# Kernel tuning notes

Hardware: AMD Instinct MI355X
Metric: run time of the kernel (lower is better)

## Reference

```python
import jax, jax.numpy as jnp
import numpy as np

NEURON_CDECAY = 0.5
NEURON_VDECAY = 0.75
NEURON_VTH = 0.5
SPIKE_PSEUDO_GRAD_WINDOW = 0.5

@jax.custom_vjp
def pseudo_spike(v):
    return (v > NEURON_VTH).astype(v.dtype)

def _ps_fwd(v):
    return pseudo_spike(v), v

def _ps_bwd(v, g):
    return (g * (jnp.abs(v - NEURON_VTH) < SPIKE_PSEUDO_GRAD_WINDOW).astype(g.dtype),)

pseudo_spike.defvjp(_ps_fwd, _ps_bwd)

def conv1d(x, w, b):
    # x: (B, Cin, L), w: (Cout, Cin, K), stride 2, VALID padding
    y = jax.lax.conv_general_dilated(x, w, window_strides=(2,), padding='VALID',
                                     dimension_numbers=('NCH', 'OIH', 'NCH'))
    return y + b[None, :, None]

def neuron(syn_out, u, v, s):
    u = u * NEURON_CDECAY + syn_out
    v = v * NEURON_VDECAY * (1.0 - s) + u
    s = pseudo_spike(v)
    return u, v, s

def setup_inputs() -> dict:
    key = jax.random.key(0)
    ks = jax.random.split(key, 18)
    B, T, L = 4096, 50, 360
    h1, h2, h3, A = 256, 256, 128, 2
    def w(k, shape, fan_in):
        bound = 1.0 / np.sqrt(fan_in)
        return jax.random.uniform(k, shape, jnp.float32, -bound, bound)
    return {
        'normal_spikes': (jax.random.uniform(ks[0], (B, 6, T)) < 0.5).astype(jnp.float32),
        'scan_spikes': (jax.random.uniform(ks[1], (B, 1, L, T)) < 0.5).astype(jnp.float32),
        'batch_size': B,
        'conv1_w': w(ks[2], (5, 1, 5), 5),   'conv1_b': w(ks[3], (5,), 5),
        'conv2_w': w(ks[4], (5, 5, 5), 25),  'conv2_b': w(ks[5], (5,), 25),
        'conv3_w': w(ks[6], (5, 5, 5), 25),  'conv3_b': w(ks[7], (5,), 25),
        'fc1_w': w(ks[8], (h1, 216), 216),   'fc1_b': w(ks[9], (h1,), 216),
        'fc2_w': w(ks[10], (h2, h1), h1),    'fc2_b': w(ks[11], (h2,), h1),
        'fc3_w': w(ks[12], (h3, h2), h2),    'fc3_b': w(ks[13], (h3,), h2),
        'fc4_w': w(ks[14], (A, h3), h3),     'fc4_b': w(ks[15], (A,), h3),
    }

def reference(normal_spikes, scan_spikes, batch_size,
              conv1_w, conv1_b, conv2_w, conv2_b, conv3_w, conv3_b,
              fc1_w, fc1_b, fc2_w, fc2_b, fc3_w, fc3_b, fc4_w, fc4_b):
    B = batch_size
    T = normal_spikes.shape[-1]
    A = fc4_w.shape[0]
    # time-major sequences for lax.scan
    scan_seq = jnp.moveaxis(scan_spikes, -1, 0)    # (T, B, 1, 360)
    norm_seq = jnp.moveaxis(normal_spikes, -1, 0)  # (T, B, 6)

    z = lambda *s: jnp.zeros(s, jnp.float32)
    init = (
        (z(B, 5, 178), z(B, 5, 178), z(B, 5, 178)),
        (z(B, 5, 87),  z(B, 5, 87),  z(B, 5, 87)),
        (z(B, 5, 42),  z(B, 5, 42),  z(B, 5, 42)),
        (z(B, 256), z(B, 256), z(B, 256)),
        (z(B, 256), z(B, 256), z(B, 256)),
        (z(B, 128), z(B, 128), z(B, 128)),
        (z(B, A),   z(B, A),   z(B, A)),
        z(B, A),
    )

    def step(carry, xs):
        c1, c2, c3, f1, f2, f3, f4, acc = carry
        scan_x, norm_x = xs
        c1 = neuron(conv1d(scan_x, conv1_w, conv1_b), *c1)
        c2 = neuron(conv1d(c1[2], conv2_w, conv2_b), *c2)
        c3 = neuron(conv1d(c2[2], conv3_w, conv3_b), *c3)
        comb = jnp.concatenate([c3[2].reshape(B, -1), norm_x], axis=1)  # (B, 216)
        f1 = neuron(comb @ fc1_w.T + fc1_b, *f1)
        f2 = neuron(f1[2] @ fc2_w.T + fc2_b, *f2)
        f3 = neuron(f2[2] @ fc3_w.T + fc3_b, *f3)
        f4 = neuron(f3[2] @ fc4_w.T + fc4_b, *f4)
        acc = acc + f4[2]
        return (c1, c2, c3, f1, f2, f3, f4, acc), None

    carry, _ = jax.lax.scan(step, init, (scan_seq, norm_seq))
    return carry[-1] / T
```

## Files before the change

### kernel.cpp

```cpp
#include <hip/hip_runtime.h>
#include <cstdint>
#include <cstddef>


#define NB 4096

__device__ __forceinline__ void neuron_update(float syn, float& u, float& v, float& s) {
    u = u * 0.5f + syn;
    v = v * 0.75f * (1.0f - s) + u;
    s = (v > 0.5f) ? 1.0f : 0.0f;
}

__global__ __launch_bounds__(192) void conv1_kernel(
    const float* __restrict__ x, const float* __restrict__ w1,
    const float* __restrict__ b1, unsigned long long* __restrict__ S1)
{
    __shared__ float xl[9000];
    const int tid = threadIdx.x;
    const int b = blockIdx.x;
    const int j = tid;
    const int lbase = (j < 178) ? 2 * j : 354;

    float wr[25], br[5];
#pragma unroll
    for (int q = 0; q < 25; ++q) wr[q] = w1[q];
#pragma unroll
    for (int o = 0; o < 5; ++o) br[o] = b1[o];

    float u[5], v[5], s[5];
#pragma unroll
    for (int o = 0; o < 5; ++o) { u[o] = 0.f; v[o] = 0.f; s[o] = 0.f; }

    const float* xb = x + (size_t)b * 18000;
    for (int half = 0; half < 2; ++half) {
        const int t0 = half * 25;
        __syncthreads();
        for (int e = tid; e < 9000; e += 192)
            xl[e] = xb[(e / 25) * 50 + t0 + (e % 25)];
        __syncthreads();
        for (int dt = 0; dt < 25; ++dt) {
            const int t = t0 + dt;
            float xv[5];
#pragma unroll
            for (int k = 0; k < 5; ++k) xv[k] = xl[(lbase + k) * 25 + dt];
#pragma unroll
            for (int o = 0; o < 5; ++o) {
                float syn = 0.f;
#pragma unroll
                for (int k = 0; k < 5; ++k) syn += wr[o * 5 + k] * xv[k];
                syn += br[o];
                neuron_update(syn, u[o], v[o], s[o]);
                unsigned long long m = __ballot(j < 178 && s[o] > 0.5f);
                if ((tid & 63) == 0)
                    S1[(((size_t)b * 50 + t) * 5 + o) * 3 + (tid >> 6)] = m;
            }
        }
    }
}

__global__ __launch_bounds__(128) void conv2_kernel(
    const unsigned int* __restrict__ S1, const float* __restrict__ w2,
    const float* __restrict__ b2, unsigned int* __restrict__ S2)
{
    __shared__ unsigned int s1l[1501];
    const int tid = threadIdx.x;
    const int b = blockIdx.x;

    float wr[125], br[5];
#pragma unroll
    for (int q = 0; q < 125; ++q) wr[q] = w2[q];
#pragma unroll
    for (int o = 0; o < 5; ++o) br[o] = b2[o];

    const unsigned int* src = S1 + (size_t)b * 1500;
    for (int e = tid; e < 1500; e += 128) s1l[e] = src[e];
    __syncthreads();

    const int p = (tid < 87) ? 2 * tid : 172;
    const int pw = p >> 5, ps = p & 31;

    float u[5], v[5], s[5];
#pragma unroll
    for (int o = 0; o < 5; ++o) { u[o] = 0.f; v[o] = 0.f; s[o] = 0.f; }

    for (int t = 0; t < 50; ++t) {
        float xv[25];
#pragma unroll
        for (int ci = 0; ci < 5; ++ci) {
            const int base = (t * 5 + ci) * 6 + pw;
            unsigned long long bits =
                ((((unsigned long long)s1l[base + 1]) << 32) | (unsigned long long)s1l[base]) >> ps;
#pragma unroll
            for (int k = 0; k < 5; ++k)
                xv[ci * 5 + k] = ((bits >> k) & 1ULL) ? 1.0f : 0.0f;
        }
#pragma unroll
        for (int o = 0; o < 5; ++o) {
            float syn = 0.f;
#pragma unroll
            for (int q = 0; q < 25; ++q) syn += wr[o * 25 + q] * xv[q];
            syn += br[o];
            neuron_update(syn, u[o], v[o], s[o]);
            unsigned long long m = __ballot(tid < 87 && s[o] > 0.5f);
            const size_t outb = (((size_t)b * 50 + t) * 5 + o) * 3;
            if (tid == 0) {
                S2[outb]     = (unsigned int)m;
                S2[outb + 1] = (unsigned int)(m >> 32);
            }
            if (tid == 64) S2[outb + 2] = (unsigned int)m;
        }
    }
}

__global__ __launch_bounds__(64) void conv3_kernel(
    const unsigned int* __restrict__ S2, const float* __restrict__ w3,
    const float* __restrict__ b3, const float* __restrict__ normal,
    unsigned long long* __restrict__ S3)
{
    __shared__ unsigned int s2l[751];
    const int tid = threadIdx.x;
    const int b = blockIdx.x;

    float wr[125], br[5];
#pragma unroll
    for (int q = 0; q < 125; ++q) wr[q] = w3[q];
#pragma unroll
    for (int o = 0; o < 5; ++o) br[o] = b3[o];

    const unsigned int* src = S2 + (size_t)b * 750;
    for (int e = tid; e < 750; e += 64) s2l[e] = src[e];
    __syncthreads();

    const int p = (tid < 42) ? 2 * tid : 82;
    const int pw = p >> 5, ps = p & 31;

    float u[5], v[5], s[5];
#pragma unroll
    for (int o = 0; o < 5; ++o) { u[o] = 0.f; v[o] = 0.f; s[o] = 0.f; }

    for (int t = 0; t < 50; ++t) {
        float xv[25];
#pragma unroll
        for (int ci = 0; ci < 5; ++ci) {
            const int base = (t * 5 + ci) * 3 + pw;
            unsigned long long bits =
                ((((unsigned long long)s2l[base + 1]) << 32) | (unsigned long long)s2l[base]) >> ps;
#pragma unroll
            for (int k = 0; k < 5; ++k)
                xv[ci * 5 + k] = ((bits >> k) & 1ULL) ? 1.0f : 0.0f;
        }
        unsigned long long m[5];
#pragma unroll
        for (int o = 0; o < 5; ++o) {
            float syn = 0.f;
#pragma unroll
            for (int q = 0; q < 25; ++q) syn += wr[o * 25 + q] * xv[q];
            syn += br[o];
            neuron_update(syn, u[o], v[o], s[o]);
            m[o] = __ballot(tid < 42 && s[o] > 0.5f);
        }
        const unsigned long long nm =
            __ballot(tid < 6 && normal[((size_t)b * 6 + tid) * 50 + t] > 0.5f);
        if (tid == 0) {
            unsigned long long r0 = m[0] | (m[1] << 42);
            unsigned long long r1 = (m[1] >> 22) | (m[2] << 20) | (m[3] << 62);
            unsigned long long r2 = (m[3] >> 2) | (m[4] << 40);
            unsigned long long r3 = (m[4] >> 24) | (nm << 18);
            unsigned long long* dst = S3 + ((size_t)b * 50 + t) * 4;
            dst[0] = r0; dst[1] = r1; dst[2] = r2; dst[3] = r3;
        }
    }
}

__global__ __launch_bounds__(256, 2) void exact_gemm_kernel(
    const uint32_t* __restrict__ bits,
    const float* __restrict__ W,
    const float* __restrict__ bias,
    float* __restrict__ syn,
    int Ntot, int KREAL, int KT, int row0)
{
    __shared__ __align__(16) float a_lds[32 * 256];
    __shared__ __align__(16) float b_lds[32 * 128];

    const int tid = threadIdx.x;
    const int m0 = blockIdx.x * 256;
    const int nbase = blockIdx.y * 128;
    const int tm = tid & 15, tn = tid >> 4;

    const uint32_t* myBits = bits + (size_t)(row0 + m0 + tid) * 8;
    const int awBase = ((((tid >> 2) & 3) << 4) | (tid >> 4)) * 4 + (tid & 3);

    const int bn = tid & 127;
    const int bk0 = (tid >> 7) * 16;
    const float* wRow = W + (size_t)(nbase + bn) * KREAL;

    float acc[16][8];
#pragma unroll
    for (int j = 0; j < 16; ++j)
#pragma unroll
        for (int r = 0; r < 8; ++r) acc[j][r] = 0.f;

    for (int kt = 0; kt < KT; ++kt) {
        const int k0 = kt * 32;

        const uint32_t wbits = myBits[kt];
        float4 bq[4];
#pragma unroll
        for (int i = 0; i < 4; ++i) {
            const int k = k0 + bk0 + i * 4;
            if (k + 3 < KREAL) {
                bq[i] = *reinterpret_cast<const float4*>(&wRow[k]);
            } else {
                float x = 0.f, y = 0.f, z = 0.f, w = 0.f;
                if (k     < KREAL) x = wRow[k];
                if (k + 1 < KREAL) y = wRow[k + 1];
                if (k + 2 < KREAL) z = wRow[k + 2];
                if (k + 3 < KREAL) w = wRow[k + 3];
                bq[i] = make_float4(x, y, z, w);
            }
        }

        __syncthreads();

#pragma unroll
        for (int kk = 0; kk < 32; ++kk)
            a_lds[kk * 256 + awBase] = ((wbits >> kk) & 1u) ? 1.0f : 0.0f;
#pragma unroll
        for (int i = 0; i < 4; ++i) {
            b_lds[(bk0 + i * 4 + 0) * 128 + bn] = bq[i].x;
            b_lds[(bk0 + i * 4 + 1) * 128 + bn] = bq[i].y;
            b_lds[(bk0 + i * 4 + 2) * 128 + bn] = bq[i].z;
            b_lds[(bk0 + i * 4 + 3) * 128 + bn] = bq[i].w;
        }
        __syncthreads();

#pragma unroll 2
        for (int kk = 0; kk < 32; ++kk) {
            float a[16];
#pragma unroll
            for (int iq = 0; iq < 4; ++iq) {
                const float4 av = *reinterpret_cast<const float4*>(
                    &a_lds[kk * 256 + (iq * 16 + tm) * 4]);
                a[iq * 4 + 0] = av.x; a[iq * 4 + 1] = av.y;
                a[iq * 4 + 2] = av.z; a[iq * 4 + 3] = av.w;
            }
            float bf[8];
            const float4 b0 = *reinterpret_cast<const float4*>(
                &b_lds[kk * 128 + tn * 8]);
            const float4 b1 = *reinterpret_cast<const float4*>(
                &b_lds[kk * 128 + tn * 8 + 4]);
            bf[0] = b0.x; bf[1] = b0.y; bf[2] = b0.z; bf[3] = b0.w;
            bf[4] = b1.x; bf[5] = b1.y; bf[6] = b1.z; bf[7] = b1.w;
#pragma unroll
            for (int j = 0; j < 16; ++j)
#pragma unroll
                for (int r = 0; r < 8; ++r)
                    acc[j][r] += a[j] * bf[r];
        }
    }

#pragma unroll
    for (int j = 0; j < 16; ++j) {
        const int m = m0 + tm * 16 + j;
        float* so = syn + (size_t)m * Ntot + nbase + tn * 8;
        float4 o0, o1;
        o0.x = acc[j][0] + bias[nbase + tn * 8 + 0];
        o0.y = acc[j][1] + bias[nbase + tn * 8 + 1];
        o0.z = acc[j][2] + bias[nbase + tn * 8 + 2];
        o0.w = acc[j][3] + bias[nbase + tn * 8 + 3];
        o1.x = acc[j][4] + bias[nbase + tn * 8 + 4];
        o1.y = acc[j][5] + bias[nbase + tn * 8 + 5];
        o1.z = acc[j][6] + bias[nbase + tn * 8 + 6];
        o1.w = acc[j][7] + bias[nbase + tn * 8 + 7];
        *reinterpret_cast<float4*>(so) = o0;
        *reinterpret_cast<float4*>(so + 4) = o1;
    }
}

template <int N>
__global__ __launch_bounds__(256) void fc_scan_kernel(
    const float* __restrict__ syn, unsigned long long* __restrict__ SF, int b0)
{
    const int tid = threadIdx.x;
    const int wid = blockIdx.x * 4 + (tid >> 6);
    const int lane = tid & 63;
    constexpr int OB = N / 64;
    const int bl = wid / OB;
    const int ob = wid - bl * OB;
    const int o = ob * 64 + lane;

    float u = 0.f, v = 0.f, s = 0.f;
    for (int t = 0; t < 50; ++t) {
        const float sv = syn[((size_t)bl * 50 + t) * N + o];
        neuron_update(sv, u, v, s);
        const unsigned long long m = __ballot(s > 0.5f);
        if (lane == 0) SF[((size_t)(b0 + bl) * 50 + t) * OB + ob] = m;
    }
}

__global__ __launch_bounds__(256) void fc4_gemm_kernel(
    const unsigned long long* __restrict__ SF3, const float* __restrict__ W,
    const float* __restrict__ bias, float* __restrict__ syn4)
{
    const int m = blockIdx.x * 256 + threadIdx.x;
    const unsigned long long w0 = SF3[(size_t)m * 2];
    const unsigned long long w1 = SF3[(size_t)m * 2 + 1];
    float a0 = 0.f, a1 = 0.f;
#pragma unroll
    for (int i = 0; i < 64; ++i) {
        const float bit = ((w0 >> i) & 1ULL) ? 1.f : 0.f;
        a0 += W[i] * bit;
        a1 += W[128 + i] * bit;
    }
#pragma unroll
    for (int i = 0; i < 64; ++i) {
        const float bit = ((w1 >> i) & 1ULL) ? 1.f : 0.f;
        a0 += W[64 + i] * bit;
        a1 += W[192 + i] * bit;
    }
    syn4[(size_t)m * 2]     = a0 + bias[0];
    syn4[(size_t)m * 2 + 1] = a1 + bias[1];
}

__global__ __launch_bounds__(64) void fc4_scan_kernel(
    const float* __restrict__ syn4, float* __restrict__ out)
{
    const int b = blockIdx.x * 64 + threadIdx.x;
    float u0 = 0.f, v0 = 0.f, s0 = 0.f, acc0 = 0.f;
    float u1 = 0.f, v1 = 0.f, s1 = 0.f, acc1 = 0.f;
    for (int t = 0; t < 50; ++t) {
        const float x0 = syn4[((size_t)b * 50 + t) * 2];
        const float x1 = syn4[((size_t)b * 50 + t) * 2 + 1];
        neuron_update(x0, u0, v0, s0); acc0 += s0;
        neuron_update(x1, u1, v1, s1); acc1 += s1;
    }
    out[b * 2]     = acc0 / 50.0f;
    out[b * 2 + 1] = acc1 / 50.0f;
}

extern "C" void kernel_launch(void* const* d_in, const int* in_sizes, int n_in,
                              void* d_out, int out_size, void* d_ws, size_t ws_size,
                              hipStream_t stream) {
    (void)in_sizes; (void)n_in; (void)out_size;
    const float* normal = (const float*)d_in[0];
    const float* xscan  = (const float*)d_in[1];
    const float* w1  = (const float*)d_in[3];
    const float* b1  = (const float*)d_in[4];
    const float* w2  = (const float*)d_in[5];
    const float* b2  = (const float*)d_in[6];
    const float* w3  = (const float*)d_in[7];
    const float* b3  = (const float*)d_in[8];
    const float* fw1 = (const float*)d_in[9];
    const float* fb1 = (const float*)d_in[10];
    const float* fw2 = (const float*)d_in[11];
    const float* fb2 = (const float*)d_in[12];
    const float* fw3 = (const float*)d_in[13];
    const float* fb3 = (const float*)d_in[14];
    const float* fw4 = (const float*)d_in[15];
    const float* fb4 = (const float*)d_in[16];
    float* out = (float*)d_out;

    char* wp = (char*)d_ws;
    size_t off = 0;
    auto take = [&](size_t bytes) -> void* {
        void* p = wp + off;
        off += (bytes + 255) & ~(size_t)255;
        return p;
    };
    unsigned long long* S1  = (unsigned long long*)take((size_t)NB * 50 * 15 * 8);
    unsigned int*       S2  = (unsigned int*)take((size_t)NB * 50 * 15 * 4);
    unsigned long long* S3  = (unsigned long long*)take((size_t)NB * 50 * 4 * 8);
    unsigned long long* SF1 = (unsigned long long*)take((size_t)NB * 50 * 4 * 8);
    unsigned long long* SF2 = (unsigned long long*)take((size_t)NB * 50 * 4 * 8);
    unsigned long long* SF3 = (unsigned long long*)take((size_t)NB * 50 * 2 * 8);
    float*              syn4 = (float*)take((size_t)NB * 50 * 2 * 4);

    int chunk = NB;
    while (chunk > 128 && off + (size_t)chunk * 50 * 256 * 4 > ws_size) chunk >>= 1;
    float* syn = (float*)take((size_t)chunk * 50 * 256 * 4);

    conv1_kernel<<<NB, 192, 0, stream>>>(xscan, w1, b1, S1);
    conv2_kernel<<<NB, 128, 0, stream>>>((const unsigned int*)S1, w2, b2, S2);
    conv3_kernel<<<NB, 64, 0, stream>>>(S2, w3, b3, normal, S3);

    for (int b0 = 0; b0 < NB; b0 += chunk) {
        exact_gemm_kernel<<<dim3(chunk * 50 / 256, 2), 256, 0, stream>>>(
            (const uint32_t*)S3, fw1, fb1, syn, 256, 216, 7, b0 * 50);
        fc_scan_kernel<256><<<chunk, 256, 0, stream>>>(syn, SF1, b0);
    }
    for (int b0 = 0; b0 < NB; b0 += chunk) {
        exact_gemm_kernel<<<dim3(chunk * 50 / 256, 2), 256, 0, stream>>>(
            (const uint32_t*)SF1, fw2, fb2, syn, 256, 256, 8, b0 * 50);
        fc_scan_kernel<256><<<chunk, 256, 0, stream>>>(syn, SF2, b0);
    }
    for (int b0 = 0; b0 < NB; b0 += chunk) {
        exact_gemm_kernel<<<dim3(chunk * 50 / 256, 1), 256, 0, stream>>>(
            (const uint32_t*)SF2, fw3, fb3, syn, 128, 256, 8, b0 * 50);
        fc_scan_kernel<128><<<chunk / 2, 256, 0, stream>>>(syn, SF3, b0);
    }
    fc4_gemm_kernel<<<NB * 50 / 256, 256, 0, stream>>>(SF3, fw4, fb4, syn4);
    fc4_scan_kernel<<<NB / 64, 64, 0, stream>>>(syn4, out);
}
```

Baseline: 1.504 ms.

## Replace LDS-tiled bit GEMM with per-row register GEMM using transposed weights and bit planes

```diff
diff --git a/kernel.cpp b/kernel.cpp
--- a/kernel.cpp
+++ b/kernel.cpp
@@ -4,6 +4,7 @@
 
 
 #define NB 4096
+#define MTOT (NB * 50)
 
 __device__ __forceinline__ void neuron_update(float syn, float& u, float& v, float& s) {
     u = u * 0.5f + syn;
@@ -115,7 +116,7 @@
 __global__ __launch_bounds__(64) void conv3_kernel(
     const unsigned int* __restrict__ S2, const float* __restrict__ w3,
     const float* __restrict__ b3, const float* __restrict__ normal,
-    unsigned long long* __restrict__ S3)
+    unsigned int* __restrict__ ST0)
 {
     __shared__ unsigned int s2l[751];
     const int tid = threadIdx.x;
@@ -162,139 +163,121 @@
         const unsigned long long nm =
             __ballot(tid < 6 && normal[((size_t)b * 6 + tid) * 50 + t] > 0.5f);
         if (tid == 0) {
-            unsigned long long r0 = m[0] | (m[1] << 42);
-            unsigned long long r1 = (m[1] >> 22) | (m[2] << 20) | (m[3] << 62);
-            unsigned long long r2 = (m[3] >> 2) | (m[4] << 40);
-            unsigned long long r3 = (m[4] >> 24) | (nm << 18);
-            unsigned long long* dst = S3 + ((size_t)b * 50 + t) * 4;
-            dst[0] = r0; dst[1] = r1; dst[2] = r2; dst[3] = r3;
-        }
-    }
-}
-
-__global__ __launch_bounds__(256, 2) void exact_gemm_kernel(
-    const uint32_t* __restrict__ bits,
-    const float* __restrict__ W,
+            const unsigned long long r0 = m[0] | (m[1] << 42);
+            const unsigned long long r1 = (m[1] >> 22) | (m[2] << 20) | (m[3] << 62);
+            const unsigned long long r2 = (m[3] >> 2) | (m[4] << 40);
+            const unsigned long long r3 = (m[4] >> 24) | (nm << 18);
+            const size_t mrow = (size_t)b * 50 + t;
+            ST0[0 * (size_t)MTOT + mrow] = (unsigned int)r0;
+            ST0[1 * (size_t)MTOT + mrow] = (unsigned int)(r0 >> 32);
+            ST0[2 * (size_t)MTOT + mrow] = (unsigned int)r1;
+            ST0[3 * (size_t)MTOT + mrow] = (unsigned int)(r1 >> 32);
+            ST0[4 * (size_t)MTOT + mrow] = (unsigned int)r2;
+            ST0[5 * (size_t)MTOT + mrow] = (unsigned int)(r2 >> 32);
+            ST0[6 * (size_t)MTOT + mrow] = (unsigned int)r3;
+        }
+    }
+}
+
+__global__ __launch_bounds__(256) void transpose_w_kernel(
+    const float* __restrict__ W, float* __restrict__ Wt, int N, int KREAL, int KPAD)
+{
+    const int idx = blockIdx.x * 256 + threadIdx.x;
+    if (idx >= KPAD * N) return;
+    const int k = idx / N, n = idx % N;
+    Wt[idx] = (k < KREAL) ? W[(size_t)n * KREAL + k] : 0.f;
+}
+
+__global__ __launch_bounds__(256) void sgemm_bits_kernel(
+    const uint32_t* __restrict__ bitsT,
+    const float* __restrict__ Wt,
     const float* __restrict__ bias,
     float* __restrict__ syn,
-    int Ntot, int KREAL, int KT, int row0)
-{
-    __shared__ __align__(16) float a_lds[32 * 256];
-    __shared__ __align__(16) float b_lds[32 * 128];
-
-    const int tid = threadIdx.x;
-    const int m0 = blockIdx.x * 256;
-    const int nbase = blockIdx.y * 128;
-    const int tm = tid & 15, tn = tid >> 4;
-
-    const uint32_t* myBits = bits + (size_t)(row0 + m0 + tid) * 8;
-    const int awBase = ((((tid >> 2) & 3) << 4) | (tid >> 4)) * 4 + (tid & 3);
-
-    const int bn = tid & 127;
-    const int bk0 = (tid >> 7) * 16;
-    const float* wRow = W + (size_t)(nbase + bn) * KREAL;
-
-    float acc[16][8];
-#pragma unroll
-    for (int j = 0; j < 16; ++j)
-#pragma unroll
-        for (int r = 0; r < 8; ++r) acc[j][r] = 0.f;
-
+    int Ntot, int KT, int row0)
+{
+    const int tid = threadIdx.x;
+    const int mloc = blockIdx.x * 256 + tid;
+    const int mg = row0 + mloc;
+    const int nbase = blockIdx.y * 32;
+
+    uint32_t aw[8];
+#pragma unroll
+    for (int w = 0; w < 8; ++w)
+        aw[w] = (w < KT) ? bitsT[(size_t)w * MTOT + mg] : 0u;
+
+    float acc[32];
+#pragma unroll
+    for (int j = 0; j < 32; ++j) acc[j] = 0.f;
+
+    const float* wt = Wt + nbase;
     for (int kt = 0; kt < KT; ++kt) {
-        const int k0 = kt * 32;
-
-        const uint32_t wbits = myBits[kt];
-        float4 bq[4];
-#pragma unroll
-        for (int i = 0; i < 4; ++i) {
-            const int k = k0 + bk0 + i * 4;
-            if (k + 3 < KREAL) {
-                bq[i] = *reinterpret_cast<const float4*>(&wRow[k]);
-            } else {
-                float x = 0.f, y = 0.f, z = 0.f, w = 0.f;
-                if (k     < KREAL) x = wRow[k];
-                if (k + 1 < KREAL) y = wRow[k + 1];
-                if (k + 2 < KREAL) z = wRow[k + 2];
-                if (k + 3 < KREAL) w = wRow[k + 3];
-                bq[i] = make_float4(x, y, z, w);
-            }
-        }
-
-        __syncthreads();
-
-#pragma unroll
-        for (int kk = 0; kk < 32; ++kk)
-            a_lds[kk * 256 + awBase] = ((wbits >> kk) & 1u) ? 1.0f : 0.0f;
-#pragma unroll
-        for (int i = 0; i < 4; ++i) {
-            b_lds[(bk0 + i * 4 + 0) * 128 + bn] = bq[i].x;
-            b_lds[(bk0 + i * 4 + 1) * 128 + bn] = bq[i].y;
-            b_lds[(bk0 + i * 4 + 2) * 128 + bn] = bq[i].z;
-            b_lds[(bk0 + i * 4 + 3) * 128 + bn] = bq[i].w;
-        }
-        __syncthreads();
-
-#pragma unroll 2
+        const uint32_t abit = aw[kt];
+        const float* wk = wt + (size_t)(kt * 32) * Ntot;
+#pragma unroll
         for (int kk = 0; kk < 32; ++kk) {
-            float a[16];
-#pragma unroll
-            for (int iq = 0; iq < 4; ++iq) {
-                const float4 av = *reinterpret_cast<const float4*>(
-                    &a_lds[kk * 256 + (iq * 16 + tm) * 4]);
-                a[iq * 4 + 0] = av.x; a[iq * 4 + 1] = av.y;
-                a[iq * 4 + 2] = av.z; a[iq * 4 + 3] = av.w;
-            }
-            float bf[8];
-            const float4 b0 = *reinterpret_cast<const float4*>(
-                &b_lds[kk * 128 + tn * 8]);
-            const float4 b1 = *reinterpret_cast<const float4*>(
-                &b_lds[kk * 128 + tn * 8 + 4]);
-            bf[0] = b0.x; bf[1] = b0.y; bf[2] = b0.z; bf[3] = b0.w;
-            bf[4] = b1.x; bf[5] = b1.y; bf[6] = b1.z; bf[7] = b1.w;
-#pragma unroll
-            for (int j = 0; j < 16; ++j)
-#pragma unroll
-                for (int r = 0; r < 8; ++r)
-                    acc[j][r] += a[j] * bf[r];
-        }
-    }
-
-#pragma unroll
-    for (int j = 0; j < 16; ++j) {
-        const int m = m0 + tm * 16 + j;
-        float* so = syn + (size_t)m * Ntot + nbase + tn * 8;
-        float4 o0, o1;
-        o0.x = acc[j][0] + bias[nbase + tn * 8 + 0];
-        o0.y = acc[j][1] + bias[nbase + tn * 8 + 1];
-        o0.z = acc[j][2] + bias[nbase + tn * 8 + 2];
-        o0.w = acc[j][3] + bias[nbase + tn * 8 + 3];
-        o1.x = acc[j][4] + bias[nbase + tn * 8 + 4];
-        o1.y = acc[j][5] + bias[nbase + tn * 8 + 5];
-        o1.z = acc[j][6] + bias[nbase + tn * 8 + 6];
-        o1.w = acc[j][7] + bias[nbase + tn * 8 + 7];
-        *reinterpret_cast<float4*>(so) = o0;
-        *reinterpret_cast<float4*>(so + 4) = o1;
-    }
-}
-
-template <int N>
-__global__ __launch_bounds__(256) void fc_scan_kernel(
-    const float* __restrict__ syn, unsigned long long* __restrict__ SF, int b0)
+            const float a = (float)((abit >> kk) & 1u);
+            const float* wr = wk + (size_t)kk * Ntot;
+#pragma unroll
+            for (int j = 0; j < 32; ++j)
+                acc[j] = fmaf(a, wr[j], acc[j]);
+        }
+    }
+
+    float* so = syn + (size_t)mloc * Ntot + nbase;
+    const float* bs = bias + nbase;
+#pragma unroll
+    for (int q = 0; q < 8; ++q) {
+        float4 ov;
+        ov.x = acc[q * 4 + 0] + bs[q * 4 + 0];
+        ov.y = acc[q * 4 + 1] + bs[q * 4 + 1];
+        ov.z = acc[q * 4 + 2] + bs[q * 4 + 2];
+        ov.w = acc[q * 4 + 3] + bs[q * 4 + 3];
+        *reinterpret_cast<float4*>(so + q * 4) = ov;
+    }
+}
+
+__global__ __launch_bounds__(256) void fc_scanT_kernel(
+    const float* __restrict__ syn,
+    uint32_t* __restrict__ SFT,
+    int b0)
+{
+    const int tid = threadIdx.x;
+    const int lane = tid & 63;
+    const int ob = tid >> 6;
+    const int bl = blockIdx.x;
+    const int o = ob * 64 + lane;
+
+    float u = 0.f, v = 0.f, s = 0.f;
+    for (int t = 0; t < 50; ++t) {
+        const float sv = syn[((size_t)bl * 50 + t) * 256 + o];
+        neuron_update(sv, u, v, s);
+        const unsigned long long m = __ballot(s > 0.5f);
+        if (lane == 0) {
+            const size_t row = (size_t)(b0 + bl) * 50 + t;
+            SFT[(size_t)(2 * ob) * MTOT + row]     = (uint32_t)m;
+            SFT[(size_t)(2 * ob + 1) * MTOT + row] = (uint32_t)(m >> 32);
+        }
+    }
+}
+
+__global__ __launch_bounds__(256) void fc_scan128_kernel(
+    const float* __restrict__ syn,
+    unsigned long long* __restrict__ SF,
+    int b0)
 {
     const int tid = threadIdx.x;
     const int wid = blockIdx.x * 4 + (tid >> 6);
     const int lane = tid & 63;
-    constexpr int OB = N / 64;
-    const int bl = wid / OB;
-    const int ob = wid - bl * OB;
+    const int bl = wid >> 1;
+    const int ob = wid & 1;
     const int o = ob * 64 + lane;
 
     float u = 0.f, v = 0.f, s = 0.f;
     for (int t = 0; t < 50; ++t) {
-        const float sv = syn[((size_t)bl * 50 + t) * N + o];
+        const float sv = syn[((size_t)bl * 50 + t) * 128 + o];
         neuron_update(sv, u, v, s);
         const unsigned long long m = __ballot(s > 0.5f);
-        if (lane == 0) SF[((size_t)(b0 + bl) * 50 + t) * OB + ob] = m;
+        if (lane == 0) SF[((size_t)(b0 + bl) * 50 + t) * 2 + ob] = m;
     }
 }
 
@@ -309,14 +292,14 @@
 #pragma unroll
     for (int i = 0; i < 64; ++i) {
         const float bit = ((w0 >> i) & 1ULL) ? 1.f : 0.f;
-        a0 += W[i] * bit;
-        a1 += W[128 + i] * bit;
+        a0 = fmaf(bit, W[i], a0);
+        a1 = fmaf(bit, W[128 + i], a1);
     }
 #pragma unroll
     for (int i = 0; i < 64; ++i) {
         const float bit = ((w1 >> i) & 1ULL) ? 1.f : 0.f;
-        a0 += W[64 + i] * bit;
-        a1 += W[192 + i] * bit;
+        a0 = fmaf(bit, W[64 + i], a0);
+        a1 = fmaf(bit, W[192 + i], a1);
     }
     syn4[(size_t)m * 2]     = a0 + bias[0];
     syn4[(size_t)m * 2 + 1] = a1 + bias[1];
@@ -367,37 +350,44 @@
         off += (bytes + 255) & ~(size_t)255;
         return p;
     };
+    float* Wt1 = (float*)take((size_t)224 * 256 * 4);
+    float* Wt2 = (float*)take((size_t)256 * 256 * 4);
+    float* Wt3 = (float*)take((size_t)256 * 128 * 4);
     unsigned long long* S1  = (unsigned long long*)take((size_t)NB * 50 * 15 * 8);
     unsigned int*       S2  = (unsigned int*)take((size_t)NB * 50 * 15 * 4);
-    unsigned long long* S3  = (unsigned long long*)take((size_t)NB * 50 * 4 * 8);
-    unsigned long long* SF1 = (unsigned long long*)take((size_t)NB * 50 * 4 * 8);
-    unsigned long long* SF2 = (unsigned long long*)take((size_t)NB * 50 * 4 * 8);
-    unsigned long long* SF3 = (unsigned long long*)take((size_t)NB * 50 * 2 * 8);
-    float*              syn4 = (float*)take((size_t)NB * 50 * 2 * 4);
+    uint32_t* ST0 = (uint32_t*)take((size_t)8 * MTOT * 4);
+    uint32_t* ST1 = (uint32_t*)take((size_t)8 * MTOT * 4);
+    uint32_t* ST2 = (uint32_t*)take((size_t)8 * MTOT * 4);
+    unsigned long long* SF3 = (unsigned long long*)take((size_t)MTOT * 2 * 8);
+    float*              syn4 = (float*)take((size_t)MTOT * 2 * 4);
 
     int chunk = NB;
     while (chunk > 128 && off + (size_t)chunk * 50 * 256 * 4 > ws_size) chunk >>= 1;
     float* syn = (float*)take((size_t)chunk * 50 * 256 * 4);
 
+    transpose_w_kernel<<<(224 * 256 + 255) / 256, 256, 0, stream>>>(fw1, Wt1, 256, 216, 224);
+    transpose_w_kernel<<<(256 * 256 + 255) / 256, 256, 0, stream>>>(fw2, Wt2, 256, 256, 256);
+    transpose_w_kernel<<<(256 * 128 + 255) / 256, 256, 0, stream>>>(fw3, Wt3, 128, 256, 256);
+
     conv1_kernel<<<NB, 192, 0, stream>>>(xscan, w1, b1, S1);
     conv2_kernel<<<NB, 128, 0, stream>>>((const unsigned int*)S1, w2, b2, S2);
-    conv3_kernel<<<NB, 64, 0, stream>>>(S2, w3, b3, normal, S3);
+    conv3_kernel<<<NB, 64, 0, stream>>>(S2, w3, b3, normal, ST0);
 
     for (int b0 = 0; b0 < NB; b0 += chunk) {
-        exact_gemm_kernel<<<dim3(chunk * 50 / 256, 2), 256, 0, stream>>>(
-            (const uint32_t*)S3, fw1, fb1, syn, 256, 216, 7, b0 * 50);
-        fc_scan_kernel<256><<<chunk, 256, 0, stream>>>(syn, SF1, b0);
+        sgemm_bits_kernel<<<dim3(chunk * 50 / 256, 8), 256, 0, stream>>>(
+            ST0, Wt1, fb1, syn, 256, 7, b0 * 50);
+        fc_scanT_kernel<<<chunk, 256, 0, stream>>>(syn, ST1, b0);
     }
     for (int b0 = 0; b0 < NB; b0 += chunk) {
-        exact_gemm_kernel<<<dim3(chunk * 50 / 256, 2), 256, 0, stream>>>(
-            (const uint32_t*)SF1, fw2, fb2, syn, 256, 256, 8, b0 * 50);
-        fc_scan_kernel<256><<<chunk, 256, 0, stream>>>(syn, SF2, b0);
+        sgemm_bits_kernel<<<dim3(chunk * 50 / 256, 8), 256, 0, stream>>>(
+            ST1, Wt2, fb2, syn, 256, 8, b0 * 50);
+        fc_scanT_kernel<<<chunk, 256, 0, stream>>>(syn, ST2, b0);
     }
     for (int b0 = 0; b0 < NB; b0 += chunk) {
-        exact_gemm_kernel<<<dim3(chunk * 50 / 256, 1), 256, 0, stream>>>(
-            (const uint32_t*)SF2, fw3, fb3, syn, 128, 256, 8, b0 * 50);
-        fc_scan_kernel<128><<<chunk / 2, 256, 0, stream>>>(syn, SF3, b0);
-    }
-    fc4_gemm_kernel<<<NB * 50 / 256, 256, 0, stream>>>(SF3, fw4, fb4, syn4);
+        sgemm_bits_kernel<<<dim3(chunk * 50 / 256, 4), 256, 0, stream>>>(
+            ST2, Wt3, fb3, syn, 128, 8, b0 * 50);
+        fc_scan128_kernel<<<chunk / 2, 256, 0, stream>>>(syn, SF3, b0);
+    }
+    fc4_gemm_kernel<<<MTOT / 256, 256, 0, stream>>>(SF3, fw4, fb4, syn4);
     fc4_scan_kernel<<<NB / 64, 64, 0, stream>>>(syn4, out);
 }
```

Result: slower. 1.609 ms (+7.0%).
